# Kernel tuning notes

Measured on AMD Instinct MI355X. Metric: run time of the kernel, lower is better.

The kernel has to match this reference:

```python
import jax, jax.numpy as jnp
import numpy as np

B, N, W, D = 32, 576, 32, 256  # batch, patches, max concepts per sample, embed dim


def _l2norm(x, eps=1e-12):
    # matches torch F.normalize: x / max(||x||, eps)
    n = jnp.linalg.norm(x, axis=-1, keepdims=True)
    return x / jnp.maximum(n, eps)


def setup_inputs() -> dict:
    key = jax.random.key(0)
    k1, k2, k3 = jax.random.split(key, 3)
    return {
        "image_token_features": jax.random.normal(k1, (B, N, D), dtype=jnp.float32),
        "concept_text_features": jax.random.normal(k2, (B, W, D), dtype=jnp.float32),
        "concept_lengths": jax.random.randint(k3, (B,), 1, W + 1, dtype=jnp.int32),
        "logit_scale": jnp.array([2.0], dtype=jnp.float32),   # log-scale, clamp(-10,10).exp()
        "logit_bias": jnp.array([-1.0], dtype=jnp.float32),
    }


def reference(image_token_features, concept_text_features, logit_scale, logit_bias, concept_lengths):
    img = _l2norm(image_token_features)          # (B, N, D)
    con = _l2norm(concept_text_features)         # (B, W, D)
    # A[m, c, n, w] = cos(patch_n of image m, concept_w of sample c)
    A = jnp.einsum('mnd,cwd->mcnw', img, con)    # (B, B, N, W) -- dominant intermediate
    max_per_concept = A.max(axis=2)              # max over patches -> (B, B, W)
    # masked mean over valid concepts (ragged lengths)
    mask = (jnp.arange(W)[None, :] < concept_lengths[:, None]).astype(img.dtype)  # (B, W)
    lens = concept_lengths.astype(img.dtype)     # all >= 1 by construction
    sim = jnp.sum(max_per_concept * mask[None, :, :], axis=-1) / lens[None, :]    # (B, B)
    t = jnp.exp(jnp.clip(logit_scale, -10.0, 10.0))[0]
    logits = jnp.clip(t * sim + logit_bias[0], -50.0, 50.0)
    z = 2.0 * jnp.eye(sim.shape[0], dtype=sim.dtype) - 1.0  # +1 diag, -1 off-diag
    loss = -jnp.mean(jax.nn.log_sigmoid(z * logits))
    return loss
```

## Files before the change

kernel.cpp:

```cpp
#include <hip/hip_runtime.h>
#include <hip/hip_bf16.h>
#include <math.h>

#define BB 32
#define NP 576
#define WW 32
#define DD 256

typedef __bf16 bf16x8 __attribute__((ext_vector_type(8)));
typedef float f32x4 __attribute__((ext_vector_type(4)));

__device__ __forceinline__ unsigned short f2bf(float f) {
  unsigned int u = __float_as_uint(f);
  u += 0x7FFFu + ((u >> 16) & 1u);
  return (unsigned short)(u >> 16);
}

__device__ __forceinline__ void gld_lds16(const unsigned short* g, unsigned short* l) {
  __builtin_amdgcn_global_load_lds(
      (const __attribute__((address_space(1))) void*)g,
      (__attribute__((address_space(3))) void*)l, 16, 0, 0);
}

__global__ __launch_bounds__(256) void norm_cast_kernel(
    const float* __restrict__ img, const float* __restrict__ con,
    unsigned short* __restrict__ img_t, unsigned short* __restrict__ con_t) {
  int row = blockIdx.x * 4 + (threadIdx.x >> 6);
  int lane = threadIdx.x & 63;
  const int n_img = BB * NP;
  const float* src;
  unsigned short* dstbase;
  int prow;
  if (row < n_img) {
    src = img + (size_t)row * DD;
    dstbase = img_t;
    prow = row;
  } else {
    prow = row - n_img;
    src = con + (size_t)prow * DD;
    dstbase = con_t;
  }
  float4 v = ((const float4*)src)[lane];
  float ss = v.x * v.x + v.y * v.y + v.z * v.z + v.w * v.w;
  #pragma unroll
  for (int off = 1; off < 64; off <<= 1) ss += __shfl_xor(ss, off);
  float inv = 1.0f / fmaxf(sqrtf(ss), 1e-12f);
  ushort4 o;
  o.x = f2bf(v.x * inv);
  o.y = f2bf(v.y * inv);
  o.z = f2bf(v.z * inv);
  o.w = f2bf(v.w * inv);
  size_t di = ((size_t)(prow >> 4) * 8 + (lane >> 3)) * 512 +
              (size_t)((((lane >> 1) & 3) * 16 + (prow & 15)) * 8) + (lane & 1) * 4;
  *(ushort4*)(dstbase + di) = o;
}

__global__ __launch_bounds__(256, 3) void gemm_max_kernel(
    const unsigned short* __restrict__ img_t,
    const unsigned short* __restrict__ con_t,
    float* __restrict__ P) {
  int bx = blockIdx.x;
  int bw = bx & 7;
  int bm = bx >> 3;
  int m = bm / 5;
  int t = bm - m * 5;
  int p0 = m * NP + t * 128;
  int w0 = bw * 128;

  __shared__ __align__(16) unsigned short ldsA[8192];
  __shared__ __align__(16) unsigned short ldsB[8192];
  __shared__ float sm[256];

  int tid = threadIdx.x;
  int wid = tid >> 6;
  int lane = tid & 63;
  int wp = wid >> 1;
  int wc = wid & 1;

  f32x4 acc[4][4];
  #pragma unroll
  for (int i = 0; i < 4; ++i)
    #pragma unroll
    for (int j = 0; j < 4; ++j) acc[i][j] = (f32x4){0.f, 0.f, 0.f, 0.f};

  const unsigned short* gA = img_t + (size_t)(p0 >> 4) * 4096 + lane * 8;
  const unsigned short* gB = con_t + (size_t)(w0 >> 4) * 4096 + lane * 8;

  for (int kb = 0; kb < 4; ++kb) {
    __syncthreads();
    #pragma unroll
    for (int u = 0; u < 4; ++u) {
      int s = wid * 4 + u;
      int gi = s >> 1;
      int kk2 = s & 1;
      size_t goff = ((size_t)gi * 8 + kb * 2 + kk2) * 512;
      gld_lds16(gA + goff, &ldsA[s * 512]);
      gld_lds16(gB + goff, &ldsB[s * 512]);
    }
    __syncthreads();
    #pragma unroll
    for (int kk = 0; kk < 2; ++kk) {
      bf16x8 af[4], bfr[4];
      #pragma unroll
      for (int pi = 0; pi < 4; ++pi)
        af[pi] = *(const bf16x8*)&ldsA[(((wp * 4 + pi) << 1) | kk) * 512 + lane * 8];
      #pragma unroll
      for (int wj = 0; wj < 4; ++wj)
        bfr[wj] = *(const bf16x8*)&ldsB[(((wc * 4 + wj) << 1) | kk) * 512 + lane * 8];
      #pragma unroll
      for (int pi = 0; pi < 4; ++pi)
        #pragma unroll
        for (int wj = 0; wj < 4; ++wj)
          acc[pi][wj] =
              __builtin_amdgcn_mfma_f32_16x16x32_bf16(af[pi], bfr[wj], acc[pi][wj], 0, 0, 0);
    }
  }

  float mxw[4];
  #pragma unroll
  for (int wj = 0; wj < 4; ++wj) {
    float v = -1e30f;
    #pragma unroll
    for (int pi = 0; pi < 4; ++pi) {
      v = fmaxf(v, fmaxf(fmaxf(acc[pi][wj][0], acc[pi][wj][1]),
                         fmaxf(acc[pi][wj][2], acc[pi][wj][3])));
    }
    v = fmaxf(v, __shfl_xor(v, 16));
    v = fmaxf(v, __shfl_xor(v, 32));
    mxw[wj] = v;
  }
  __syncthreads();
  if (lane < 16) {
    #pragma unroll
    for (int wj = 0; wj < 4; ++wj)
      sm[wp * 128 + wc * 64 + wj * 16 + lane] = mxw[wj];
  }
  __syncthreads();
  if (tid < 128) {
    float v = sm[tid];
    if (t != 4) v = fmaxf(v, sm[128 + tid]);
    P[(size_t)bm * 1024 + w0 + tid] = v;
  }
}

__global__ __launch_bounds__(256) void reduce_kernel(
    const float* __restrict__ P, const int* __restrict__ lengths,
    float* __restrict__ sims) {
  int pair = blockIdx.x * 4 + (threadIdx.x >> 6);
  int lane = threadIdx.x & 63;
  int m = pair >> 5;
  int c = pair & 31;
  int w = lane & 31;
  const float* base = P + (size_t)(m * 5) * 1024 + c * 32 + w;
  float v = base[0];
  v = fmaxf(v, base[1024]);
  v = fmaxf(v, base[2048]);
  v = fmaxf(v, base[3072]);
  v = fmaxf(v, base[4096]);
  int len = lengths[c];
  float contrib = (w < len) ? v : 0.0f;
  #pragma unroll
  for (int off = 1; off < 32; off <<= 1) contrib += __shfl_xor(contrib, off);
  if (lane == 0) sims[pair] = contrib / (float)len;
}

__global__ __launch_bounds__(256) void loss_kernel(
    const float* __restrict__ sims, const float* __restrict__ lscale,
    const float* __restrict__ lbias, float* __restrict__ out) {
  float tt = expf(fminf(fmaxf(lscale[0], -10.0f), 10.0f));
  float bias = lbias[0];
  int tid = threadIdx.x;
  float acc = 0.0f;
  for (int p = tid; p < BB * BB; p += 256) {
    int mm = p >> 5;
    int cc = p & 31;
    float lg = fminf(fmaxf(tt * sims[p] + bias, -50.0f), 50.0f);
    float x = (mm == cc) ? lg : -lg;
    float ls = (x >= 0.0f) ? -log1pf(expf(-x)) : (x - log1pf(expf(x)));
    acc += ls;
  }
  #pragma unroll
  for (int off = 1; off < 64; off <<= 1) acc += __shfl_xor(acc, off);
  __shared__ float s[4];
  if ((tid & 63) == 0) s[tid >> 6] = acc;
  __syncthreads();
  if (tid == 0) out[0] = -(s[0] + s[1] + s[2] + s[3]) / (float)(BB * BB);
}

extern "C" void kernel_launch(void* const* d_in, const int* in_sizes, int n_in,
                              void* d_out, int out_size, void* d_ws, size_t ws_size,
                              hipStream_t stream) {
  const float* img = (const float*)d_in[0];
  const float* con = (const float*)d_in[1];
  const int* lens = (const int*)d_in[2];
  const float* lsc = (const float*)d_in[3];
  const float* lbi = (const float*)d_in[4];

  unsigned short* img_t = (unsigned short*)d_ws;
  unsigned short* con_t = img_t + (size_t)BB * NP * DD;
  float* P = (float*)(con_t + (size_t)BB * WW * DD);
  float* sims = P + (size_t)160 * 1024;

  norm_cast_kernel<<<(BB * NP + BB * WW) / 4, 256, 0, stream>>>(img, con, img_t, con_t);
  gemm_max_kernel<<<160 * 8, 256, 0, stream>>>(img_t, con_t, P);
  reduce_kernel<<<256, 256, 0, stream>>>(P, lens, sims);
  loss_kernel<<<1, 256, 0, stream>>>(sims, lsc, lbi, (float*)d_out);
}
```

Baseline: 99.06 us.

## Fuse patch-tile max via atomics, load B fragments directly to registers

```diff
diff --git a/kernel.cpp b/kernel.cpp
--- a/kernel.cpp
+++ b/kernel.cpp
@@ -22,9 +22,22 @@
       (__attribute__((address_space(3))) void*)l, 16, 0, 0);
 }
 
+__device__ __forceinline__ unsigned int encf(float f) {
+  unsigned int b = __float_as_uint(f);
+  return (b & 0x80000000u) ? ~b : (b | 0x80000000u);
+}
+__device__ __forceinline__ float decf(unsigned int u) {
+  unsigned int b = (u & 0x80000000u) ? (u & 0x7FFFFFFFu) : ~u;
+  return __uint_as_float(b);
+}
+
 __global__ __launch_bounds__(256) void norm_cast_kernel(
     const float* __restrict__ img, const float* __restrict__ con,
-    unsigned short* __restrict__ img_t, unsigned short* __restrict__ con_t) {
+    unsigned short* __restrict__ img_t, unsigned short* __restrict__ con_t,
+    unsigned int* __restrict__ sraw) {
+  int gid = blockIdx.x * 256 + threadIdx.x;
+  if (gid < BB * 1024) sraw[gid] = 0u;
+
   int row = blockIdx.x * 4 + (threadIdx.x >> 6);
   int lane = threadIdx.x & 63;
   const int n_img = BB * NP;
@@ -58,7 +71,7 @@
 __global__ __launch_bounds__(256, 3) void gemm_max_kernel(
     const unsigned short* __restrict__ img_t,
     const unsigned short* __restrict__ con_t,
-    float* __restrict__ P) {
+    unsigned int* __restrict__ sraw) {
   int bx = blockIdx.x;
   int bw = bx & 7;
   int bm = bx >> 3;
@@ -68,7 +81,6 @@
   int w0 = bw * 128;
 
   __shared__ __align__(16) unsigned short ldsA[8192];
-  __shared__ __align__(16) unsigned short ldsB[8192];
   __shared__ float sm[256];
 
   int tid = threadIdx.x;
@@ -84,7 +96,7 @@
     for (int j = 0; j < 4; ++j) acc[i][j] = (f32x4){0.f, 0.f, 0.f, 0.f};
 
   const unsigned short* gA = img_t + (size_t)(p0 >> 4) * 4096 + lane * 8;
-  const unsigned short* gB = con_t + (size_t)(w0 >> 4) * 4096 + lane * 8;
+  const unsigned short* gB = con_t + ((size_t)(w0 >> 4) + wc * 4) * 4096 + lane * 8;
 
   for (int kb = 0; kb < 4; ++kb) {
     __syncthreads();
@@ -93,26 +105,28 @@
       int s = wid * 4 + u;
       int gi = s >> 1;
       int kk2 = s & 1;
-      size_t goff = ((size_t)gi * 8 + kb * 2 + kk2) * 512;
-      gld_lds16(gA + goff, &ldsA[s * 512]);
-      gld_lds16(gB + goff, &ldsB[s * 512]);
+      gld_lds16(gA + ((size_t)gi * 8 + kb * 2 + kk2) * 512, &ldsA[s * 512]);
     }
+    bf16x8 bfr[4][2];
+    #pragma unroll
+    for (int wj = 0; wj < 4; ++wj)
+      #pragma unroll
+      for (int kk = 0; kk < 2; ++kk)
+        bfr[wj][kk] =
+            *(const bf16x8*)(gB + ((size_t)wj * 8 + kb * 2 + kk) * 512);
     __syncthreads();
     #pragma unroll
     for (int kk = 0; kk < 2; ++kk) {
-      bf16x8 af[4], bfr[4];
+      bf16x8 af[4];
       #pragma unroll
       for (int pi = 0; pi < 4; ++pi)
         af[pi] = *(const bf16x8*)&ldsA[(((wp * 4 + pi) << 1) | kk) * 512 + lane * 8];
       #pragma unroll
-      for (int wj = 0; wj < 4; ++wj)
-        bfr[wj] = *(const bf16x8*)&ldsB[(((wc * 4 + wj) << 1) | kk) * 512 + lane * 8];
-      #pragma unroll
       for (int pi = 0; pi < 4; ++pi)
         #pragma unroll
         for (int wj = 0; wj < 4; ++wj)
-          acc[pi][wj] =
-              __builtin_amdgcn_mfma_f32_16x16x32_bf16(af[pi], bfr[wj], acc[pi][wj], 0, 0, 0);
+          acc[pi][wj] = __builtin_amdgcn_mfma_f32_16x16x32_bf16(
+              af[pi], bfr[wj][kk], acc[pi][wj], 0, 0, 0);
     }
   }
 
@@ -121,10 +135,9 @@
   for (int wj = 0; wj < 4; ++wj) {
     float v = -1e30f;
     #pragma unroll
-    for (int pi = 0; pi < 4; ++pi) {
+    for (int pi = 0; pi < 4; ++pi)
       v = fmaxf(v, fmaxf(fmaxf(acc[pi][wj][0], acc[pi][wj][1]),
                          fmaxf(acc[pi][wj][2], acc[pi][wj][3])));
-    }
     v = fmaxf(v, __shfl_xor(v, 16));
     v = fmaxf(v, __shfl_xor(v, 32));
     mxw[wj] = v;
@@ -139,52 +152,38 @@
   if (tid < 128) {
     float v = sm[tid];
     if (t != 4) v = fmaxf(v, sm[128 + tid]);
-    P[(size_t)bm * 1024 + w0 + tid] = v;
-  }
-}
-
-__global__ __launch_bounds__(256) void reduce_kernel(
-    const float* __restrict__ P, const int* __restrict__ lengths,
-    float* __restrict__ sims) {
-  int pair = blockIdx.x * 4 + (threadIdx.x >> 6);
-  int lane = threadIdx.x & 63;
-  int m = pair >> 5;
-  int c = pair & 31;
-  int w = lane & 31;
-  const float* base = P + (size_t)(m * 5) * 1024 + c * 32 + w;
-  float v = base[0];
-  v = fmaxf(v, base[1024]);
-  v = fmaxf(v, base[2048]);
-  v = fmaxf(v, base[3072]);
-  v = fmaxf(v, base[4096]);
-  int len = lengths[c];
-  float contrib = (w < len) ? v : 0.0f;
-  #pragma unroll
-  for (int off = 1; off < 32; off <<= 1) contrib += __shfl_xor(contrib, off);
-  if (lane == 0) sims[pair] = contrib / (float)len;
-}
-
-__global__ __launch_bounds__(256) void loss_kernel(
-    const float* __restrict__ sims, const float* __restrict__ lscale,
-    const float* __restrict__ lbias, float* __restrict__ out) {
-  float tt = expf(fminf(fmaxf(lscale[0], -10.0f), 10.0f));
-  float bias = lbias[0];
+    atomicMax(&sraw[(size_t)m * 1024 + w0 + tid], encf(v));
+  }
+}
+
+__global__ __launch_bounds__(1024) void loss_kernel(
+    const unsigned int* __restrict__ sraw, const int* __restrict__ lens,
+    const float* __restrict__ lsc, const float* __restrict__ lbi,
+    float* __restrict__ out) {
   int tid = threadIdx.x;
-  float acc = 0.0f;
-  for (int p = tid; p < BB * BB; p += 256) {
-    int mm = p >> 5;
-    int cc = p & 31;
-    float lg = fminf(fmaxf(tt * sims[p] + bias, -50.0f), 50.0f);
-    float x = (mm == cc) ? lg : -lg;
-    float ls = (x >= 0.0f) ? -log1pf(expf(-x)) : (x - log1pf(expf(x)));
-    acc += ls;
-  }
+  int m = tid >> 5;
+  int c = tid & 31;
+  int len = lens[c];
+  const unsigned int* base = sraw + (size_t)m * 1024 + c * 32;
+  float s = 0.0f;
+  for (int w = 0; w < WW; ++w)
+    if (w < len) s += decf(base[w]);
+  s /= (float)len;
+  float tt = expf(fminf(fmaxf(lsc[0], -10.0f), 10.0f));
+  float lg = fminf(fmaxf(tt * s + lbi[0], -50.0f), 50.0f);
+  float x = (m == c) ? lg : -lg;
+  float acc = (x >= 0.0f) ? -log1pf(expf(-x)) : (x - log1pf(expf(x)));
   #pragma unroll
   for (int off = 1; off < 64; off <<= 1) acc += __shfl_xor(acc, off);
-  __shared__ float s[4];
-  if ((tid & 63) == 0) s[tid >> 6] = acc;
+  __shared__ float sred[16];
+  if ((tid & 63) == 0) sred[tid >> 6] = acc;
   __syncthreads();
-  if (tid == 0) out[0] = -(s[0] + s[1] + s[2] + s[3]) / (float)(BB * BB);
+  if (tid == 0) {
+    float tot = 0.0f;
+    #pragma unroll
+    for (int i = 0; i < 16; ++i) tot += sred[i];
+    out[0] = -tot / (float)(BB * BB);
+  }
 }
 
 extern "C" void kernel_launch(void* const* d_in, const int* in_sizes, int n_in,
@@ -198,11 +197,10 @@
 
   unsigned short* img_t = (unsigned short*)d_ws;
   unsigned short* con_t = img_t + (size_t)BB * NP * DD;
-  float* P = (float*)(con_t + (size_t)BB * WW * DD);
-  float* sims = P + (size_t)160 * 1024;
-
-  norm_cast_kernel<<<(BB * NP + BB * WW) / 4, 256, 0, stream>>>(img, con, img_t, con_t);
-  gemm_max_kernel<<<160 * 8, 256, 0, stream>>>(img_t, con_t, P);
-  reduce_kernel<<<256, 256, 0, stream>>>(P, lens, sims);
-  loss_kernel<<<1, 256, 0, stream>>>(sims, lsc, lbi, (float*)d_out);
-}
+  unsigned int* sraw = (unsigned int*)(con_t + (size_t)BB * WW * DD);
+
+  norm_cast_kernel<<<(BB * NP + BB * WW) / 4, 256, 0, stream>>>(img, con, img_t,
+                                                                con_t, sraw);
+  gemm_max_kernel<<<160 * 8, 256, 0, stream>>>(img_t, con_t, sraw);
+  loss_kernel<<<1, 1024, 0, stream>>>(sraw, lens, lsc, lbi, (float*)d_out);
+}
```

New measurement: 102.5 us. 3.5% more time.
